# Kernel optimization log

Measured on AMD Instinct MI355X. Metric: run time of the kernel, lower is better.

Reference implementation:

```python
import jax, jax.numpy as jnp
import numpy as np

NUM_USER = 50000
NUM_ITEM = 50000
DIM_FEAT = 4096
DIM_LATENT = 128
NUM_LAYER = 2
AVG_DEG = 16
N = NUM_USER + NUM_ITEM
E_HALF = NUM_USER * AVG_DEG  # user->item edges; reversed copies added too


def setup_inputs() -> dict:
    key = jax.random.key(0)
    ks = jax.random.split(key, 6)
    features = jax.random.normal(ks[0], (NUM_ITEM, DIM_FEAT), dtype=jnp.float32)
    # xavier_normal for preference: std = sqrt(2/(fan_in+fan_out))
    preference = jax.random.normal(ks[1], (NUM_USER, DIM_LATENT), dtype=jnp.float32) * np.sqrt(2.0 / (NUM_USER + DIM_LATENT)).astype(np.float32)
    W1 = jax.random.normal(ks[2], (DIM_FEAT, 4 * DIM_LATENT), dtype=jnp.float32) * np.float32(DIM_FEAT ** -0.5)
    b1 = jnp.zeros((4 * DIM_LATENT,), jnp.float32)
    W2 = jax.random.normal(ks[3], (4 * DIM_LATENT, DIM_LATENT), dtype=jnp.float32) * np.float32((4 * DIM_LATENT) ** -0.5)
    b2 = jnp.zeros((DIM_LATENT,), jnp.float32)
    # bipartite user-item edges, both directions; no self-loops by construction
    u = jax.random.randint(ks[4], (E_HALF,), 0, NUM_USER)
    it = jax.random.randint(ks[5], (E_HALF,), NUM_USER, N)
    src = jnp.concatenate([u, it])
    dst = jnp.concatenate([it, u])
    edge_index = jnp.stack([src, dst], axis=0)
    return {"features": features, "preference": preference, "W1": W1, "b1": b1,
            "W2": W2, "b2": b2, "edge_index": edge_index}


def reference(features, preference, W1, b1, W2, b2, edge_index):
    # proj MLP: Linear -> LeakyReLU(0.01) -> Linear
    item_feat = jax.nn.leaky_relu(features @ W1 + b1, negative_slope=0.01) @ W2 + b2
    x = jnp.concatenate([preference, item_feat], axis=0)  # [N, D]
    # F.normalize(x, dim=-1): divide by L2 norm clamped to 1e-12
    x = x / jnp.maximum(jnp.linalg.norm(x, axis=-1, keepdims=True), 1e-12)
    row, col = edge_index[0], edge_index[1]  # source (j), target (i)
    # degree over source index only, as in BaseGCN.message
    deg = jax.ops.segment_sum(jnp.ones(row.shape[0], dtype=x.dtype), row, num_segments=N)
    deg_inv_sqrt = deg ** -0.5  # endpoints all appear as sources, so finite on edges
    norm = deg_inv_sqrt[row] * deg_inv_sqrt[col]  # [E]
    out = x
    h = x
    for _ in range(NUM_LAYER):
        msg = norm[:, None] * h[row]                      # gather + scale [E, D]
        h = jax.ops.segment_sum(msg, col, num_segments=N)  # scatter-add [N, D]
        out = out + h
    return out, preference
```

## Files before the change

### kernel.cpp

```cpp
#include <hip/hip_runtime.h>

#define NUSER 50000
#define NITEM 50000
#define NTOT  100000
#define DFEAT 4096
#define DLAT  128
#define DHID  512
#define MTILES 391
#define MPAD  (MTILES*128)
#define G1TILES 782

typedef __attribute__((ext_vector_type(8))) short bf16x8;
typedef __attribute__((ext_vector_type(4))) float f32x4;

__device__ __forceinline__ ushort f2bf(float f) {
  union { float f; unsigned u; } in; in.f = f;
  unsigned u = in.u;
  u += 0x7fffu + ((u >> 16) & 1u);
  return (ushort)(u >> 16);
}
__device__ __forceinline__ unsigned pk2bf_fast(float lo, float hi) {
  unsigned ul = __float_as_uint(lo) + 0x8000u;
  unsigned uh = __float_as_uint(hi) + 0x8000u;
  return (ul >> 16) | (uh & 0xffff0000u);
}
__device__ __forceinline__ float bflo(unsigned u) { return __uint_as_float(u << 16); }
__device__ __forceinline__ float bfhi(unsigned u) { return __uint_as_float(u & 0xffff0000u); }

__global__ __launch_bounds__(512, 4) void gemm1_kernel(
    const float* __restrict__ A,
    const ushort* __restrict__ BT,
    const float* __restrict__ bias,
    ushort* __restrict__ Hid)
{
  extern __shared__ char smem[];
  char* AsC = smem;
  char* BsC = smem + 8192;

  const int tid = threadIdx.x;
  const int lane = tid & 63;
  const int wid = tid >> 6;
  const int row0 = blockIdx.x * 64;

  const int lr = lane & 15;
  const int kq = lane >> 4;
  const int l7 = lane & 7;

  f32x4 acc[4][4];
  const f32x4 z = {0.f, 0.f, 0.f, 0.f};
  #pragma unroll
  for (int m = 0; m < 4; ++m)
    #pragma unroll
    for (int n = 0; n < 4; ++n) acc[m][n] = z;

  const int r0 = tid >> 3, t0 = tid & 7;
  const int aoff = r0 * 128 + ((t0 ^ (r0 & 7)) << 4);
  const float* aptr = A + (size_t)min(row0 + r0, NITEM - 1) * DFEAT + t0 * 8;

  for (int k0 = 0; k0 < DFEAT; k0 += 64) {
    #pragma unroll
    for (int j = 0; j < 8; ++j) {
      int q = (wid * 8 + j) * 64 + lane;
      int r = q >> 3, t = q & 7;
      const ushort* src = BT + (size_t)r * DFEAT + k0 + ((t ^ (r & 7)) << 3);
      __builtin_amdgcn_global_load_lds(
          (const __attribute__((address_space(1))) void*)src,
          (__attribute__((address_space(3))) void*)(BsC + (size_t)(wid * 8 + j) * 1024),
          16, 0, 0);
    }
    {
      const float* s = aptr + k0;
      float4 v0 = *(const float4*)s;
      float4 v1 = *(const float4*)(s + 4);
      uint4 p;
      p.x = pk2bf_fast(v0.x, v0.y); p.y = pk2bf_fast(v0.z, v0.w);
      p.z = pk2bf_fast(v1.x, v1.y); p.w = pk2bf_fast(v1.z, v1.w);
      *(uint4*)(AsC + aoff) = p;
    }
    __syncthreads();

    #pragma unroll
    for (int kk = 0; kk < 2; ++kk) {
      const int c8 = kk * 4 + kq;
      const int sx = (c8 ^ l7) << 4;
      bf16x8 a[4];
      #pragma unroll
      for (int m = 0; m < 4; ++m)
        a[m] = *(const bf16x8*)(AsC + (m * 16 + lr) * 128 + sx);
      #pragma unroll
      for (int n = 0; n < 4; ++n) {
        bf16x8 b = *(const bf16x8*)(BsC + (wid * 64 + n * 16 + lr) * 128 + sx);
        #pragma unroll
        for (int m = 0; m < 4; ++m)
          acc[m][n] = __builtin_amdgcn_mfma_f32_16x16x32_bf16(a[m], b, acc[m][n], 0, 0, 0);
      }
    }
    __syncthreads();
  }

  #pragma unroll
  for (int n = 0; n < 4; ++n) {
    int col = wid * 64 + n * 16 + lr;
    float bv = bias[col];
    #pragma unroll
    for (int m = 0; m < 4; ++m) {
      #pragma unroll
      for (int i = 0; i < 4; ++i) {
        int row = row0 + m * 16 + kq * 4 + i;
        float v = acc[m][n][i] + bv;
        v = v > 0.f ? v : 0.01f * v;
        Hid[(size_t)row * DHID + col] = f2bf(v);
      }
    }
  }
}

#define BM 128
#define BK 32
#define LDW 40

__global__ __launch_bounds__(256, 4) void gemm2_kernel(
    const ushort* __restrict__ A,
    const ushort* __restrict__ BT,
    const float* __restrict__ bias,
    float* __restrict__ X,
    unsigned* __restrict__ Xb)
{
  __shared__ ushort As[BM][LDW];
  __shared__ ushort Bs[BM][LDW];
  __shared__ float rsum[BM];
  const int tid = threadIdx.x;
  const int lane = tid & 63;
  const int wid = tid >> 6;
  const int wr = wid >> 1, wc = wid & 1;
  const int row0 = blockIdx.x * BM;

  f32x4 acc[4][4];
  const f32x4 z = {0.f, 0.f, 0.f, 0.f};
  #pragma unroll
  for (int m = 0; m < 4; ++m)
    #pragma unroll
    for (int n = 0; n < 4; ++n) acc[m][n] = z;

  const int lrow = lane & 15;
  const int kq = lane >> 4;
  const int kb = kq * 8;

  for (int k0 = 0; k0 < DHID; k0 += BK) {
    #pragma unroll
    for (int j = 0; j < 2; ++j) {
      int idx = tid + j * 256;
      int r = idx >> 2;
      int c8 = (idx & 3) << 3;
      *(uint4*)&As[r][c8] = *(const uint4*)(A + (size_t)(row0 + r) * DHID + k0 + c8);
      *(uint4*)&Bs[r][c8] = *(const uint4*)(BT + (size_t)r * DHID + k0 + c8);
    }
    __syncthreads();
    bf16x8 a[4], b[4];
    #pragma unroll
    for (int m = 0; m < 4; ++m) a[m] = *(const bf16x8*)&As[wr * 64 + m * 16 + lrow][kb];
    #pragma unroll
    for (int n = 0; n < 4; ++n) b[n] = *(const bf16x8*)&Bs[wc * 64 + n * 16 + lrow][kb];
    #pragma unroll
    for (int m = 0; m < 4; ++m)
      #pragma unroll
      for (int n = 0; n < 4; ++n)
        acc[m][n] = __builtin_amdgcn_mfma_f32_16x16x32_bf16(a[m], b[n], acc[m][n], 0, 0, 0);
    __syncthreads();
  }

  float prt[4][4];
  #pragma unroll
  for (int m = 0; m < 4; ++m)
    #pragma unroll
    for (int i = 0; i < 4; ++i) prt[m][i] = 0.f;
  #pragma unroll
  for (int n = 0; n < 4; ++n) {
    float bv = bias[wc * 64 + n * 16 + lrow];
    #pragma unroll
    for (int m = 0; m < 4; ++m)
      #pragma unroll
      for (int i = 0; i < 4; ++i) {
        float v = acc[m][n][i] + bv;
        prt[m][i] += v * v;
      }
  }
  #pragma unroll
  for (int msk = 1; msk < 16; msk <<= 1)
    #pragma unroll
    for (int m = 0; m < 4; ++m)
      #pragma unroll
      for (int i = 0; i < 4; ++i)
        prt[m][i] += __shfl_xor(prt[m][i], msk, 64);
  if (wc == 0 && lrow == 0) {
    #pragma unroll
    for (int m = 0; m < 4; ++m)
      #pragma unroll
      for (int i = 0; i < 4; ++i)
        rsum[wr * 64 + m * 16 + kq * 4 + i] = prt[m][i];
  }
  __syncthreads();
  if (wc == 1 && lrow == 0) {
    #pragma unroll
    for (int m = 0; m < 4; ++m)
      #pragma unroll
      for (int i = 0; i < 4; ++i)
        rsum[wr * 64 + m * 16 + kq * 4 + i] += prt[m][i];
  }
  __syncthreads();

  #pragma unroll
  for (int n = 0; n < 4; ++n) {
    int col = wc * 64 + n * 16 + lrow;
    float bv = bias[col];
    #pragma unroll
    for (int m = 0; m < 4; ++m) {
      #pragma unroll
      for (int i = 0; i < 4; ++i) {
        int rl = wr * 64 + m * 16 + kq * 4 + i;
        int row = row0 + rl;
        float inv = rsqrtf(fmaxf(rsum[rl], 1e-24f));
        float v = (acc[m][n][i] + bv) * inv;
        float vo = __shfl_xor(v, 1, 64);
        if (row < NITEM) {
          size_t node = (size_t)(NUSER + row);
          X[node * DLAT + col] = v;
          if ((lrow & 1) == 0)
            Xb[node * 64 + (col >> 1)] = pk2bf_fast(v, vo);
        }
      }
    }
  }
}

__global__ __launch_bounds__(256) void prep_w1t(const float* __restrict__ W1,
                                                ushort* __restrict__ W1T) {
  __shared__ ushort t[64][72];
  const int bx = blockIdx.x & 63;
  const int by = blockIdx.x >> 6;
  const int k0 = bx * 64, n0 = by * 64;
  const int tid = threadIdx.x;
  #pragma unroll
  for (int j = 0; j < 4; ++j) {
    int f = tid + j * 256;
    int r = f >> 4, c4 = (f & 15) << 2;
    float4 v = *(const float4*)(W1 + (size_t)(k0 + r) * DHID + n0 + c4);
    t[c4 + 0][r] = f2bf(v.x);
    t[c4 + 1][r] = f2bf(v.y);
    t[c4 + 2][r] = f2bf(v.z);
    t[c4 + 3][r] = f2bf(v.w);
  }
  __syncthreads();
  #pragma unroll
  for (int j = 0; j < 2; ++j) {
    int o = tid + j * 256;
    int r = o >> 3, c8 = (o & 7) << 3;
    *(uint4*)(W1T + (size_t)(n0 + r) * DFEAT + k0 + c8) = *(const uint4*)&t[r][c8];
  }
}
__global__ void prep_w2t(const float* __restrict__ W2, ushort* __restrict__ W2T) {
  int idx = blockIdx.x * 256 + threadIdx.x;
  int n = idx >> 9, k = idx & 511;
  W2T[idx] = f2bf(W2[(size_t)k * DLAT + n]);
}

__global__ __launch_bounds__(256) void normalize_pref(
    const float* __restrict__ pref, float* __restrict__ X,
    unsigned* __restrict__ Xb) {
  int gw = (blockIdx.x * 256 + threadIdx.x) >> 6;
  int lane = threadIdx.x & 63;
  if (gw >= NUSER) return;
  float2 v = *(const float2*)(pref + (size_t)gw * DLAT + lane * 2);
  float s = v.x * v.x + v.y * v.y;
  #pragma unroll
  for (int off = 32; off; off >>= 1) s += __shfl_xor(s, off, 64);
  float inv = 1.0f / fmaxf(sqrtf(s), 1e-12f);
  float2 o; o.x = v.x * inv; o.y = v.y * inv;
  *(float2*)(X + (size_t)gw * DLAT + lane * 2) = o;
  Xb[(size_t)gw * 64 + lane] = pk2bf_fast(o.x, o.y);
}

__global__ void count_kernel(const int* __restrict__ col, int* __restrict__ cnt, int E) {
  int e = blockIdx.x * 256 + threadIdx.x;
  if (e < E) atomicAdd(&cnt[col[e]], 1);
}
__global__ void dinv_kernel(const int* __restrict__ cnt, float* __restrict__ dinv, int n) {
  int i = blockIdx.x * 256 + threadIdx.x;
  if (i < n) dinv[i] = rsqrtf((float)cnt[i]);
}

#define SCAN_NB ((NTOT + 1023) / 1024)
__global__ __launch_bounds__(1024) void scan1_kernel(const int* __restrict__ cnt,
                                                     int* __restrict__ off,
                                                     int* __restrict__ bsum, int n) {
  __shared__ int ws[16];
  __shared__ int wexcl[16];
  const int tid = threadIdx.x, lane = tid & 63, wv = tid >> 6;
  int i = blockIdx.x * 1024 + tid;
  int v = (i < n) ? cnt[i] : 0;
  int x = v;
  #pragma unroll
  for (int o = 1; o < 64; o <<= 1) {
    int t = __shfl_up(x, o, 64);
    if (lane >= o) x += t;
  }
  if (lane == 63) ws[wv] = x;
  __syncthreads();
  if (tid < 16) {
    int y = ws[tid];
    #pragma unroll
    for (int o = 1; o < 16; o <<= 1) {
      int t = __shfl_up(y, o, 64);
      if (tid >= o) y += t;
    }
    wexcl[tid] = y - ws[tid];
    if (tid == 15) bsum[blockIdx.x] = y;
  }
  __syncthreads();
  if (i < n) off[i] = wexcl[wv] + (x - v);
}
__global__ __launch_bounds__(128) void scan2_kernel(int* __restrict__ bsum,
                                                    int* __restrict__ off, int nb, int n) {
  __shared__ int ws[2];
  const int tid = threadIdx.x, lane = tid & 63, wv = tid >> 6;
  int v = (tid < nb) ? bsum[tid] : 0;
  int x = v;
  #pragma unroll
  for (int o = 1; o < 64; o <<= 1) {
    int t = __shfl_up(x, o, 64);
    if (lane >= o) x += t;
  }
  if (lane == 63) ws[wv] = x;
  __syncthreads();
  int excl_w = (wv == 1) ? ws[0] : 0;
  if (tid < nb) bsum[tid] = excl_w + (x - v);
  if (tid == nb - 1) off[n] = excl_w + x;
}
__global__ __launch_bounds__(1024) void scan3_kernel(int* __restrict__ off,
                                                     const int* __restrict__ bsum, int n) {
  int i = blockIdx.x * 1024 + threadIdx.x;
  if (i < n) off[i] += bsum[blockIdx.x];
}

__global__ void fill_kernel(const int* __restrict__ row, const int* __restrict__ col,
                            const float* __restrict__ dinv, const int* __restrict__ off,
                            int* __restrict__ cur, int2* __restrict__ srcw, int E) {
  int e = blockIdx.x * 256 + threadIdx.x;
  if (e >= E) return;
  int r = row[e], c = col[e];
  float w = dinv[r] * dinv[c];
  int p = atomicAdd(&cur[c], 1);
  int2 pk; pk.x = r; pk.y = __float_as_int(w);
  srcw[off[c] + p] = pk;
}

template <int FINAL>
__global__ __launch_bounds__(256) void spmm_kernel(
    const int2* __restrict__ srcw, const int* __restrict__ off,
    const unsigned* __restrict__ hb, float* __restrict__ hout,
    unsigned* __restrict__ houtb,
    const float* __restrict__ addX, const unsigned* __restrict__ addH1) {
  int node = (int)((blockIdx.x * 256 + threadIdx.x) >> 6);
  int lane = threadIdx.x & 63;
  if (node >= NTOT) return;
  int p = off[node], pend = off[node + 1];
  float ax = 0.f, ay = 0.f;
  for (; p + 3 < pend; p += 4) {
    int2 e0 = srcw[p];
    int2 e1 = srcw[p + 1];
    int2 e2 = srcw[p + 2];
    int2 e3 = srcw[p + 3];
    unsigned u0 = hb[(size_t)e0.x * 64 + lane];
    unsigned u1 = hb[(size_t)e1.x * 64 + lane];
    unsigned u2 = hb[(size_t)e2.x * 64 + lane];
    unsigned u3 = hb[(size_t)e3.x * 64 + lane];
    float w0 = __int_as_float(e0.y), w1 = __int_as_float(e1.y);
    float w2 = __int_as_float(e2.y), w3 = __int_as_float(e3.y);
    ax += w0 * bflo(u0) + w1 * bflo(u1) + w2 * bflo(u2) + w3 * bflo(u3);
    ay += w0 * bfhi(u0) + w1 * bfhi(u1) + w2 * bfhi(u2) + w3 * bfhi(u3);
  }
  for (; p < pend; ++p) {
    int2 e0 = srcw[p];
    float w0 = __int_as_float(e0.y);
    unsigned u0 = hb[(size_t)e0.x * 64 + lane];
    ax += w0 * bflo(u0);
    ay += w0 * bfhi(u0);
  }
  if (FINAL) {
    size_t o = (size_t)node * DLAT + lane * 2;
    float2 a = *(const float2*)(addX + o);
    unsigned h1 = addH1[(size_t)node * 64 + lane];
    ax += a.x + bflo(h1);
    ay += a.y + bfhi(h1);
    float2 r; r.x = ax; r.y = ay;
    *(float2*)(hout + o) = r;
  } else {
    houtb[(size_t)node * 64 + lane] = pk2bf_fast(ax, ay);
  }
}

extern "C" void kernel_launch(void* const* d_in, const int* in_sizes, int n_in,
                              void* d_out, int out_size, void* d_ws, size_t ws_size,
                              hipStream_t stream) {
  const float* features  = (const float*)d_in[0];
  const float* preference = (const float*)d_in[1];
  const float* W1 = (const float*)d_in[2];
  const float* b1 = (const float*)d_in[3];
  const float* W2 = (const float*)d_in[4];
  const float* b2 = (const float*)d_in[5];
  const int*   edges = (const int*)d_in[6];
  const int E = in_sizes[6] / 2;
  const int* erow = edges;
  const int* ecol = edges + E;
  float* out = (float*)d_out;

  char* ws = (char*)d_ws;
  size_t off_b = 0;
  auto alloc = [&](size_t bytes) {
    void* p = ws + off_b;
    off_b = (off_b + bytes + 255) & ~(size_t)255;
    return p;
  };
  ushort*   W1T  = (ushort*)alloc((size_t)DHID * DFEAT * 2);
  ushort*   W2T  = (ushort*)alloc((size_t)DLAT * DHID * 2);
  ushort*   Hid  = (ushort*)alloc((size_t)MPAD * DHID * 2);
  float*    X    = (float*)alloc((size_t)NTOT * DLAT * 4);
  unsigned* Xb   = (unsigned*)alloc((size_t)NTOT * 64 * 4);
  unsigned* hAb  = (unsigned*)alloc((size_t)NTOT * 64 * 4);
  int*      cnt  = (int*)alloc((size_t)NTOT * 4);
  int*      offs = (int*)alloc((size_t)(NTOT + 1) * 4);
  int*      cur  = (int*)alloc((size_t)NTOT * 4);
  float*    dinv = (float*)alloc((size_t)NTOT * 4);
  int*      bsum = (int*)alloc((size_t)SCAN_NB * 4);
  int2*     srcw = (int2*)alloc((size_t)E * 8);

  prep_w1t<<<512, 256, 0, stream>>>(W1, W1T);
  prep_w2t<<<(DLAT * DHID) / 256, 256, 0, stream>>>(W2, W2T);
  gemm1_kernel<<<G1TILES, 512, 72 * 1024, stream>>>(features, W1T, b1, Hid);
  gemm2_kernel<<<MTILES, 256, 0, stream>>>(Hid, W2T, b2, X, Xb);
  normalize_pref<<<(NUSER * 64 + 255) / 256, 256, 0, stream>>>(preference, X, Xb);

  hipMemsetAsync(cnt, 0, (size_t)NTOT * 4, stream);
  count_kernel<<<(E + 255) / 256, 256, 0, stream>>>(ecol, cnt, E);
  dinv_kernel<<<(NTOT + 255) / 256, 256, 0, stream>>>(cnt, dinv, NTOT);
  scan1_kernel<<<SCAN_NB, 1024, 0, stream>>>(cnt, offs, bsum, NTOT);
  scan2_kernel<<<1, 128, 0, stream>>>(bsum, offs, SCAN_NB, NTOT);
  scan3_kernel<<<SCAN_NB, 1024, 0, stream>>>(offs, bsum, NTOT);
  hipMemsetAsync(cur, 0, (size_t)NTOT * 4, stream);
  fill_kernel<<<(E + 255) / 256, 256, 0, stream>>>(erow, ecol, dinv, offs, cur, srcw, E);

  spmm_kernel<0><<<(NTOT * 64 + 255) / 256, 256, 0, stream>>>(srcw, offs, Xb, nullptr, hAb, nullptr, nullptr);
  spmm_kernel<1><<<(NTOT * 64 + 255) / 256, 256, 0, stream>>>(srcw, offs, hAb, out, nullptr, X, hAb);

  hipMemcpyAsync(out + (size_t)NTOT * DLAT, preference, (size_t)NUSER * DLAT * 4,
                 hipMemcpyDeviceToDevice, stream);
}
```

Measured before the change: 747.1 us.

## Fuse second MLP GEMM and row normalization into first GEMM kernel

Merges the hidden-layer GEMM and the output projection into one kernel. The LeakyReLU hidden tile is written as bf16 into shared memory (swizzled) instead of global memory, then multiplied by W2T read directly from global, followed by an in-block L2 row normalization. This removes the global round-trip of the hidden activation and one kernel launch. In exchange, the second GEMM now runs per 64-row tile with W2 fetched from global/cache by every block.

After: 749.7 us. No clear change (+0.3%).

```diff
diff --git a/kernel.cpp b/kernel.cpp
--- a/kernel.cpp
+++ b/kernel.cpp
@@ -6,8 +6,6 @@
 #define DFEAT 4096
 #define DLAT  128
 #define DHID  512
-#define MTILES 391
-#define MPAD  (MTILES*128)
 #define G1TILES 782
 
 typedef __attribute__((ext_vector_type(8))) short bf16x8;
@@ -27,15 +25,19 @@
 __device__ __forceinline__ float bflo(unsigned u) { return __uint_as_float(u << 16); }
 __device__ __forceinline__ float bfhi(unsigned u) { return __uint_as_float(u & 0xffff0000u); }
 
-__global__ __launch_bounds__(512, 4) void gemm1_kernel(
+__global__ __launch_bounds__(512, 4) void mlp_kernel(
     const float* __restrict__ A,
-    const ushort* __restrict__ BT,
-    const float* __restrict__ bias,
-    ushort* __restrict__ Hid)
+    const ushort* __restrict__ W1T,
+    const float* __restrict__ b1,
+    const ushort* __restrict__ W2T,
+    const float* __restrict__ b2,
+    float* __restrict__ X,
+    unsigned* __restrict__ Xb)
 {
   extern __shared__ char smem[];
   char* AsC = smem;
   char* BsC = smem + 8192;
+  float* rsumW = (float*)AsC;
 
   const int tid = threadIdx.x;
   const int lane = tid & 63;
@@ -62,7 +64,7 @@
     for (int j = 0; j < 8; ++j) {
       int q = (wid * 8 + j) * 64 + lane;
       int r = q >> 3, t = q & 7;
-      const ushort* src = BT + (size_t)r * DFEAT + k0 + ((t ^ (r & 7)) << 3);
+      const ushort* src = W1T + (size_t)r * DFEAT + k0 + ((t ^ (r & 7)) << 3);
       __builtin_amdgcn_global_load_lds(
           (const __attribute__((address_space(1))) void*)src,
           (__attribute__((address_space(3))) void*)(BsC + (size_t)(wid * 8 + j) * 1024),
@@ -83,17 +85,18 @@
     for (int kk = 0; kk < 2; ++kk) {
       const int c8 = kk * 4 + kq;
       const int sx = (c8 ^ l7) << 4;
-      bf16x8 a[4];
+      bf16x8 a[4], b[4];
       #pragma unroll
       for (int m = 0; m < 4; ++m)
         a[m] = *(const bf16x8*)(AsC + (m * 16 + lr) * 128 + sx);
       #pragma unroll
-      for (int n = 0; n < 4; ++n) {
-        bf16x8 b = *(const bf16x8*)(BsC + (wid * 64 + n * 16 + lr) * 128 + sx);
+      for (int n = 0; n < 4; ++n)
+        b[n] = *(const bf16x8*)(BsC + (wid * 64 + n * 16 + lr) * 128 + sx);
+      #pragma unroll
+      for (int m = 0; m < 4; ++m)
         #pragma unroll
-        for (int m = 0; m < 4; ++m)
-          acc[m][n] = __builtin_amdgcn_mfma_f32_16x16x32_bf16(a[m], b, acc[m][n], 0, 0, 0);
-      }
+        for (int n = 0; n < 4; ++n)
+          acc[m][n] = __builtin_amdgcn_mfma_f32_16x16x32_bf16(a[m], b[n], acc[m][n], 0, 0, 0);
     }
     __syncthreads();
   }
@@ -101,90 +104,50 @@
   #pragma unroll
   for (int n = 0; n < 4; ++n) {
     int col = wid * 64 + n * 16 + lr;
-    float bv = bias[col];
-    #pragma unroll
-    for (int m = 0; m < 4; ++m) {
+    float bv = b1[col];
+    #pragma unroll
+    for (int m = 0; m < 4; ++m)
       #pragma unroll
       for (int i = 0; i < 4; ++i) {
-        int row = row0 + m * 16 + kq * 4 + i;
         float v = acc[m][n][i] + bv;
         v = v > 0.f ? v : 0.01f * v;
-        Hid[(size_t)row * DHID + col] = f2bf(v);
+        float vo = __shfl_xor(v, 1, 64);
+        if (!(lr & 1)) {
+          int row = m * 16 + kq * 4 + i;
+          int s = col >> 3;
+          int sw = (s & 56) | ((s & 7) ^ (row & 7));
+          *(unsigned*)(BsC + row * 1024 + sw * 16 + ((col * 2) & 15)) = pk2bf_fast(v, vo);
+        }
       }
-    }
-  }
-}
-
-#define BM 128
-#define BK 32
-#define LDW 40
-
-__global__ __launch_bounds__(256, 4) void gemm2_kernel(
-    const ushort* __restrict__ A,
-    const ushort* __restrict__ BT,
-    const float* __restrict__ bias,
-    float* __restrict__ X,
-    unsigned* __restrict__ Xb)
-{
-  __shared__ ushort As[BM][LDW];
-  __shared__ ushort Bs[BM][LDW];
-  __shared__ float rsum[BM];
-  const int tid = threadIdx.x;
-  const int lane = tid & 63;
-  const int wid = tid >> 6;
-  const int wr = wid >> 1, wc = wid & 1;
-  const int row0 = blockIdx.x * BM;
-
-  f32x4 acc[4][4];
-  const f32x4 z = {0.f, 0.f, 0.f, 0.f};
+  }
+  __syncthreads();
+
+  f32x4 acc2[4];
+  #pragma unroll
+  for (int m = 0; m < 4; ++m) acc2[m] = z;
+  const ushort* w2p = W2T + (size_t)(wid * 16 + lr) * DHID;
+  #pragma unroll
+  for (int ks = 0; ks < 16; ++ks) {
+    bf16x8 b = *(const bf16x8*)(w2p + ks * 32 + kq * 8);
+    #pragma unroll
+    for (int m = 0; m < 4; ++m) {
+      int row = m * 16 + lr;
+      int s = ks * 4 + kq;
+      int sw = (s & 56) | ((s & 7) ^ (row & 7));
+      bf16x8 a = *(const bf16x8*)(BsC + row * 1024 + sw * 16);
+      acc2[m] = __builtin_amdgcn_mfma_f32_16x16x32_bf16(a, b, acc2[m], 0, 0, 0);
+    }
+  }
+
+  const float bv2 = b2[wid * 16 + lr];
+  float prt[4][4];
   #pragma unroll
   for (int m = 0; m < 4; ++m)
     #pragma unroll
-    for (int n = 0; n < 4; ++n) acc[m][n] = z;
-
-  const int lrow = lane & 15;
-  const int kq = lane >> 4;
-  const int kb = kq * 8;
-
-  for (int k0 = 0; k0 < DHID; k0 += BK) {
-    #pragma unroll
-    for (int j = 0; j < 2; ++j) {
-      int idx = tid + j * 256;
-      int r = idx >> 2;
-      int c8 = (idx & 3) << 3;
-      *(uint4*)&As[r][c8] = *(const uint4*)(A + (size_t)(row0 + r) * DHID + k0 + c8);
-      *(uint4*)&Bs[r][c8] = *(const uint4*)(BT + (size_t)r * DHID + k0 + c8);
-    }
-    __syncthreads();
-    bf16x8 a[4], b[4];
-    #pragma unroll
-    for (int m = 0; m < 4; ++m) a[m] = *(const bf16x8*)&As[wr * 64 + m * 16 + lrow][kb];
-    #pragma unroll
-    for (int n = 0; n < 4; ++n) b[n] = *(const bf16x8*)&Bs[wc * 64 + n * 16 + lrow][kb];
-    #pragma unroll
-    for (int m = 0; m < 4; ++m)
-      #pragma unroll
-      for (int n = 0; n < 4; ++n)
-        acc[m][n] = __builtin_amdgcn_mfma_f32_16x16x32_bf16(a[m], b[n], acc[m][n], 0, 0, 0);
-    __syncthreads();
-  }
-
-  float prt[4][4];
-  #pragma unroll
-  for (int m = 0; m < 4; ++m)
-    #pragma unroll
-    for (int i = 0; i < 4; ++i) prt[m][i] = 0.f;
-  #pragma unroll
-  for (int n = 0; n < 4; ++n) {
-    float bv = bias[wc * 64 + n * 16 + lrow];
-    #pragma unroll
-    for (int m = 0; m < 4; ++m)
-      #pragma unroll
-      for (int i = 0; i < 4; ++i) {
-        float v = acc[m][n][i] + bv;
-        prt[m][i] += v * v;
-      }
-  }
+    for (int i = 0; i < 4; ++i) {
+      float v = acc2[m][i] + bv2;
+      prt[m][i] = v * v;
+    }
   #pragma unroll
   for (int msk = 1; msk < 16; msk <<= 1)
     #pragma unroll
@@ -192,45 +155,39 @@
       #pragma unroll
       for (int i = 0; i < 4; ++i)
         prt[m][i] += __shfl_xor(prt[m][i], msk, 64);
-  if (wc == 0 && lrow == 0) {
+  if (lr == 0) {
     #pragma unroll
     for (int m = 0; m < 4; ++m)
       #pragma unroll
       for (int i = 0; i < 4; ++i)
-        rsum[wr * 64 + m * 16 + kq * 4 + i] = prt[m][i];
-  }
-  __syncthreads();
-  if (wc == 1 && lrow == 0) {
-    #pragma unroll
-    for (int m = 0; m < 4; ++m)
-      #pragma unroll
-      for (int i = 0; i < 4; ++i)
-        rsum[wr * 64 + m * 16 + kq * 4 + i] += prt[m][i];
-  }
-  __syncthreads();
-
-  #pragma unroll
-  for (int n = 0; n < 4; ++n) {
-    int col = wc * 64 + n * 16 + lrow;
-    float bv = bias[col];
-    #pragma unroll
-    for (int m = 0; m < 4; ++m) {
-      #pragma unroll
-      for (int i = 0; i < 4; ++i) {
-        int rl = wr * 64 + m * 16 + kq * 4 + i;
-        int row = row0 + rl;
-        float inv = rsqrtf(fmaxf(rsum[rl], 1e-24f));
-        float v = (acc[m][n][i] + bv) * inv;
-        float vo = __shfl_xor(v, 1, 64);
-        if (row < NITEM) {
-          size_t node = (size_t)(NUSER + row);
-          X[node * DLAT + col] = v;
-          if ((lrow & 1) == 0)
-            Xb[node * 64 + (col >> 1)] = pk2bf_fast(v, vo);
-        }
+        rsumW[wid * 64 + m * 16 + kq * 4 + i] = prt[m][i];
+  }
+  __syncthreads();
+  if (tid < 64) {
+    float s = 0.f;
+    #pragma unroll
+    for (int w = 0; w < 8; ++w) s += rsumW[w * 64 + tid];
+    rsumW[tid] = s;
+  }
+  __syncthreads();
+
+  #pragma unroll
+  for (int m = 0; m < 4; ++m)
+    #pragma unroll
+    for (int i = 0; i < 4; ++i) {
+      int rl = m * 16 + kq * 4 + i;
+      int grow = row0 + rl;
+      float inv = rsqrtf(fmaxf(rsumW[rl], 1e-24f));
+      float v = (acc2[m][i] + bv2) * inv;
+      float vo = __shfl_xor(v, 1, 64);
+      if (grow < NITEM) {
+        size_t node = (size_t)(NUSER + grow);
+        int col = wid * 16 + lr;
+        X[node * DLAT + col] = v;
+        if (!(lr & 1))
+          Xb[node * 64 + (col >> 1)] = pk2bf_fast(v, vo);
       }
     }
-  }
 }
 
 __global__ __launch_bounds__(256) void prep_w1t(const float* __restrict__ W1,
@@ -423,7 +380,6 @@
   };
   ushort*   W1T  = (ushort*)alloc((size_t)DHID * DFEAT * 2);
   ushort*   W2T  = (ushort*)alloc((size_t)DLAT * DHID * 2);
-  ushort*   Hid  = (ushort*)alloc((size_t)MPAD * DHID * 2);
   float*    X    = (float*)alloc((size_t)NTOT * DLAT * 4);
   unsigned* Xb   = (unsigned*)alloc((size_t)NTOT * 64 * 4);
   unsigned* hAb  = (unsigned*)alloc((size_t)NTOT * 64 * 4);
@@ -436,8 +392,7 @@
 
   prep_w1t<<<512, 256, 0, stream>>>(W1, W1T);
   prep_w2t<<<(DLAT * DHID) / 256, 256, 0, stream>>>(W2, W2T);
-  gemm1_kernel<<<G1TILES, 512, 72 * 1024, stream>>>(features, W1T, b1, Hid);
-  gemm2_kernel<<<MTILES, 256, 0, stream>>>(Hid, W2T, b2, X, Xb);
+  mlp_kernel<<<G1TILES, 512, 72 * 1024, stream>>>(features, W1T, b1, W2T, b2, X, Xb);
   normalize_pref<<<(NUSER * 64 + 255) / 256, 256, 0, stream>>>(preference, X, Xb);
 
   hipMemsetAsync(cnt, 0, (size_t)NTOT * 4, stream);
```
